# Kernel optimization log

Hardware: AMD Instinct MI355X
Metric: run time of the kernel (lower is better)

## Reference

```python
import jax, jax.numpy as jnp
import numpy as np

N_NODES = 15000
N_EDGES = 300000
N_RADIAL = 8
N_SPEC = 16
ZMAX = 64
CUTOFF = 5.0
LMAX = 2
NCHANNELS = 128


def bessel_basis(r, dim, rc):
    # b_n(r) = sqrt(2/rc) * sin(n*pi*r/rc) / r , n = 1..dim
    n = jnp.arange(1, dim + 1, dtype=r.dtype)
    return jnp.sqrt(2.0 / rc) * jnp.sin(n[None, :] * (jnp.pi / rc) * r[:, None]) / r[:, None]


def spherical_harmonics_l2(u):
    # Real solid harmonics of unit vectors up to l=2 (Racah/L2-style constants), 9 components
    x, y, z = u[:, 0], u[:, 1], u[:, 2]
    s3 = 3.0 ** 0.5
    s5 = 5.0 ** 0.5
    s15 = 15.0 ** 0.5
    one = jnp.ones_like(x)
    return jnp.stack([
        one,
        s3 * x, s3 * y, s3 * z,
        s15 * x * y, s15 * y * z,
        0.5 * s5 * (3.0 * z * z - 1.0),
        s15 * x * z, 0.5 * s15 * (x * x - y * y),
    ], axis=-1)  # [E, 9]


def setup_inputs() -> dict:
    key = jax.random.key(0)
    ks = jax.random.split(key, 8)
    vec = jax.random.normal(ks[0], (N_EDGES, 3), dtype=jnp.float32)
    distances = jnp.linalg.norm(vec, axis=-1) + 1e-3  # positive, consistent with vec
    switch = jax.random.uniform(ks[1], (N_EDGES,), dtype=jnp.float32)
    species_table = jax.random.normal(ks[2], (ZMAX, N_SPEC), dtype=jnp.float32)
    nbasis = N_RADIAL * N_SPEC
    W0 = jax.random.normal(ks[3], (nbasis, 2 * NCHANNELS), dtype=jnp.float32) / jnp.sqrt(nbasis)
    W1 = jax.random.normal(ks[4], (nbasis, 2 * NCHANNELS), dtype=jnp.float32) / jnp.sqrt(nbasis)
    W2 = jax.random.normal(ks[5], (nbasis, 2 * NCHANNELS), dtype=jnp.float32) / jnp.sqrt(nbasis)
    species = jax.random.randint(ks[6], (N_NODES,), 0, ZMAX)
    edge_src = jnp.sort(jax.random.randint(ks[7], (N_EDGES,), 0, N_NODES))
    edge_dst = jax.random.randint(jax.random.fold_in(key, 7), (N_EDGES,), 0, N_NODES)
    return {
        "distances": distances, "vec": vec, "switch": switch,
        "species_table": species_table, "W0": W0, "W1": W1, "W2": W2,
        "species": species, "edge_src": edge_src, "edge_dst": edge_dst,
    }


def reference(distances, vec, switch, species_table, W0, W1, W2, species, edge_src, edge_dst):
    n_nodes = species.shape[0]
    # radial basis * switch: [E, nr]
    rb = bessel_basis(distances, N_RADIAL, CUTOFF) * switch[:, None]
    senc = species_table[species]  # [N, ns]
    # edge-wise outer product radial x species -> [E, nr*ns]
    Dij = (rb[:, :, None] * senc[edge_dst, None, :]).reshape(rb.shape[0], -1)
    Y = spherical_harmonics_l2(vec / distances[:, None])  # [E, 9]
    # outer product with SH then scatter-sum to nodes: [N, 9, nbasis]
    rhoi = jax.ops.segment_sum(Dij[:, None, :] * Y[:, :, None], edge_src, num_segments=n_nodes)
    xis = [senc, rhoi[:, 0, :]]
    for l, W in enumerate((W0, W1, W2)):
        rhoil = rhoi[:, l * l:(l + 1) * (l + 1), :]  # [N, 2l+1, nbasis]
        xy = jnp.einsum('nmb,bc->nmc', rhoil, W)      # [N, 2l+1, 2*nchannels]
        xl, yl = jnp.split(xy, 2, axis=-1)
        xis.append((xl * yl).sum(axis=1) / (2 * l + 1) ** 0.5)
    return jnp.concatenate(xis, axis=-1)  # [N, ns + nbasis + 3*nchannels]
```

## Files before the change

kernel.cpp:

```cpp
#include <hip/hip_runtime.h>
#include <math.h>

#define N_NODES 15000
#define NPAD    15008
#define N_EDGES 300000
#define NCH     128
#define OUT_COLS 528
#define ES      300032
#define NCHUNK  (ES / 32)
#define CHROWS  72

typedef _Float16 half8   __attribute__((ext_vector_type(8)));
typedef short    short8  __attribute__((ext_vector_type(8)));
typedef float    floatx4 __attribute__((ext_vector_type(4)));

#define WF_BYTES    (3 * 256 * 128 * 2)
#define RP_OFF      WF_BYTES
#define RP_BYTES    61440
#define SPE_OFF     (RP_OFF + RP_BYTES)
#define SPE_BYTES   ((size_t)ES * 2)
#define AYT_OFF     (SPE_OFF + SPE_BYTES)
#define AYT_BYTES   ((size_t)NCHUNK * CHROWS * 32 * 2 + 4096)

#define PREP_EDGE_BLOCKS 1172
#define PREP_WF_BLOCKS   384
#define PREP_RP_BLOCKS   59
#define PREP_BLOCKS (PREP_EDGE_BLOCKS + PREP_WF_BLOCKS + PREP_RP_BLOCKS)

__device__ __forceinline__ size_t wf_pos(int l, int c, int k) {
    int h = c >> 7, cc = c & 127;
    int ct = cc >> 4, nI = cc & 15;
    int K = k >> 5, q = (k >> 3) & 3, j = k & 7;
    return ((size_t)((((l * 8 + ct) * 2 + h) * 4 + K) * 64 + q * 16 + nI)) * 8 + j;
}

__global__ __launch_bounds__(256) void prep_kernel(
    const float* __restrict__ dist, const float* __restrict__ vec,
    const float* __restrict__ sw,   const int* __restrict__ species,
    const int* __restrict__ edst,   const int* __restrict__ esrc,
    const float* __restrict__ W0, const float* __restrict__ W1,
    const float* __restrict__ W2,
    _Float16* __restrict__ AYt, short* __restrict__ spE,
    _Float16* __restrict__ WF,  int* __restrict__ row_ptr)
{
    const int b = blockIdx.x, tid = threadIdx.x;
    if (b < PREP_EDGE_BLOCKS) {
        int e = b * 256 + tid;
        if (e >= N_EDGES) return;

        const float bnorm = 0.6324555320336759f;
        const float s3  = 1.7320508075688772f;
        const float s5  = 2.2360679774997896f;
        const float s15 = 3.872983346207417f;
        const float cstep = 3.14159265358979323846f / 5.0f;

        float r    = dist[e];
        float invr = 1.0f / r;
        float g    = bnorm * invr * sw[e];
        float x = vec[3*e+0] * invr;
        float y = vec[3*e+1] * invr;
        float z = vec[3*e+2] * invr;

        spE[e] = (short)species[edst[e]];

        float f[8];
        #pragma unroll
        for (int n = 0; n < 8; ++n)
            f[n] = g * __sinf((float)(n + 1) * cstep * r);

        float Y[9];
        Y[0] = 1.0f;
        Y[1] = s3 * x;  Y[2] = s3 * y;  Y[3] = s3 * z;
        Y[4] = s15 * x * y;  Y[5] = s15 * y * z;
        Y[6] = 0.5f * s5 * (3.0f * z * z - 1.0f);
        Y[7] = s15 * x * z;  Y[8] = 0.5f * s15 * (x * x - y * y);

        _Float16* ab = AYt + (size_t)(e >> 5) * (CHROWS * 32) + (e & 31);
        #pragma unroll
        for (int m = 0; m < 9; ++m)
            #pragma unroll
            for (int n = 0; n < 8; ++n)
                ab[(m * 8 + n) * 32] = (_Float16)(Y[m] * f[n]);
    } else if (b < PREP_EDGE_BLOCKS + PREP_WF_BLOCKS) {
        int idx = (b - PREP_EDGE_BLOCKS) * 256 + tid;
        int l = idx >> 15;
        int c = (idx >> 7) & 255;
        int k = idx & 127;
        const float* W = (l == 0) ? W0 : ((l == 1) ? W1 : W2);
        WF[wf_pos(l, c, k)] = (_Float16)W[k * 256 + c];
    } else {
        int i = (b - PREP_EDGE_BLOCKS - PREP_WF_BLOCKS) * 256 + tid;
        if (i > NPAD) return;
        int lo = 0, hi = N_EDGES;
        while (lo < hi) { int mid = (lo + hi) >> 1; if (esrc[mid] < i) lo = mid + 1; else hi = mid; }
        row_ptr[i] = lo;
    }
}

__global__ __launch_bounds__(256) void main_kernel(
    const _Float16* __restrict__ AYt, const short* __restrict__ spE,
    const float* __restrict__ stab,  const int* __restrict__ row_ptr,
    const _Float16* __restrict__ WF, const int* __restrict__ species,
    float* __restrict__ out)
{
    __shared__ _Float16 stabL[64 * 16];
    __shared__ __align__(16) _Float16 srho[144 * 136];

    const int tid  = threadIdx.x;
    const int wave = tid >> 6;
    const int lane = tid & 63;
    const int q    = lane >> 4;
    const int nI   = lane & 15;
    const int node0 = blockIdx.x * 16;

    #pragma unroll
    for (int j = 0; j < 4; ++j) stabL[tid * 4 + j] = (_Float16)stab[tid * 4 + j];
    __syncthreads();

    for (int i = 0; i < 4; ++i) {
        const int n16 = 4 * wave + i;
        const int node = node0 + n16;
        const int lo = row_ptr[node], hi = row_ptr[node + 1];

        floatx4 acc[5];
        #pragma unroll
        for (int t = 0; t < 5; ++t) acc[t] = (floatx4){0.f, 0.f, 0.f, 0.f};

        for (int k0 = (lo & ~31); k0 < hi; k0 += 32) {
            short8 sp8 = *(const short8*)(spE + k0 + q * 8);
            half8 bfr;
            #pragma unroll
            for (int j = 0; j < 8; ++j) {
                int e = k0 + q * 8 + j;
                bool valid = (e >= lo) && (e < hi);
                int spv = valid ? (int)sp8[j] : 0;
                _Float16 v = stabL[spv * 16 + nI];
                bfr[j] = valid ? v : (_Float16)0;
            }
            const _Float16* cb = AYt + (size_t)(k0 >> 5) * (CHROWS * 32) + q * 8;
            #pragma unroll
            for (int t = 0; t < 5; ++t) {
                half8 a = *(const half8*)(cb + (t * 16 + nI) * 32);
                acc[t] = __builtin_amdgcn_mfma_f32_16x16x32_f16(a, bfr, acc[t], 0, 0, 0);
            }
        }

        #pragma unroll
        for (int t = 0; t < 5; ++t)
            #pragma unroll
            for (int r = 0; r < 4; ++r) {
                int row = t * 16 + q * 4 + r;
                if (row < 72) {
                    int m = row >> 3, nrad = row & 7;
                    int k = nrad * 16 + nI;
                    int K = k >> 5, qq = (k >> 3) & 3, j = k & 7;
                    srho[((m * 4 + K) * 4 + qq) * 136 + n16 * 8 + j] = (_Float16)acc[t][r];
                }
            }
    }
    __syncthreads();

    {
        int nn = tid >> 4, c = tid & 15;
        int node = node0 + nn;
        if (node < N_NODES) {
            float* o = out + (size_t)node * OUT_COLS;
            o[c] = stab[species[node] * 16 + c];
            int c0 = c * 8;
            int K = c0 >> 5, qq = (c0 >> 3) & 3;
            half8 h = *(const half8*)&srho[(K * 4 + qq) * 136 + nn * 8];
            #pragma unroll
            for (int j = 0; j < 8; ++j) o[16 + c0 + j] = (float)h[j];
        }
    }

    const int   mstart[3] = {0, 1, 4};
    const int   mcount[3] = {1, 3, 5};
    const float scl[3] = {1.0f, 0.5773502691896258f, 0.4472135954999579f};

    #pragma unroll
    for (int l = 0; l < 3; ++l) {
        half8 Bf[2][2][4];
        #pragma unroll
        for (int cp = 0; cp < 2; ++cp)
            #pragma unroll
            for (int h = 0; h < 2; ++h) {
                int ct = 2 * wave + cp;
                const _Float16* bp = WF +
                    ((size_t)((((l * 8 + ct) * 2 + h) * 4) * 64 + lane)) * 8;
                #pragma unroll
                for (int K = 0; K < 4; ++K)
                    Bf[cp][h][K] = *(const half8*)(bp + (size_t)K * 512);
            }

        floatx4 P0 = {0.f, 0.f, 0.f, 0.f};
        floatx4 P1 = {0.f, 0.f, 0.f, 0.f};

        #pragma unroll
        for (int mi = 0; mi < mcount[l]; ++mi) {
            int m = mstart[l] + mi;
            half8 Af[4];
            #pragma unroll
            for (int K = 0; K < 4; ++K)
                Af[K] = *(const half8*)&srho[((m * 4 + K) * 4 + q) * 136 + nI * 8];

            #pragma unroll
            for (int cp = 0; cp < 2; ++cp) {
                floatx4 Cx = {0.f, 0.f, 0.f, 0.f};
                floatx4 Cy = {0.f, 0.f, 0.f, 0.f};
                #pragma unroll
                for (int K = 0; K < 4; ++K) {
                    Cx = __builtin_amdgcn_mfma_f32_16x16x32_f16(Af[K], Bf[cp][0][K], Cx, 0, 0, 0);
                    Cy = __builtin_amdgcn_mfma_f32_16x16x32_f16(Af[K], Bf[cp][1][K], Cy, 0, 0, 0);
                }
                if (cp == 0) P0 += Cx * Cy; else P1 += Cx * Cy;
            }
        }

        #pragma unroll
        for (int cp = 0; cp < 2; ++cp) {
            floatx4 P = cp ? P1 : P0;
            int c = 144 + l * NCH + 16 * (2 * wave + cp) + nI;
            #pragma unroll
            for (int r = 0; r < 4; ++r) {
                int node = node0 + q * 4 + r;
                if (node < N_NODES)
                    out[(size_t)node * OUT_COLS + c] = P[r] * scl[l];
            }
        }
    }
}

extern "C" void kernel_launch(void* const* d_in, const int* in_sizes, int n_in,
                              void* d_out, int out_size, void* d_ws, size_t ws_size,
                              hipStream_t stream) {
    const float* distances = (const float*)d_in[0];
    const float* vec       = (const float*)d_in[1];
    const float* sw        = (const float*)d_in[2];
    const float* stab      = (const float*)d_in[3];
    const float* W0        = (const float*)d_in[4];
    const float* W1        = (const float*)d_in[5];
    const float* W2        = (const float*)d_in[6];
    const int*   species   = (const int*)d_in[7];
    const int*   esrc      = (const int*)d_in[8];
    const int*   edst      = (const int*)d_in[9];
    float* out = (float*)d_out;

    _Float16* WF     = (_Float16*)d_ws;
    int*      rowptr = (int*)((char*)d_ws + RP_OFF);
    short*    spE    = (short*)((char*)d_ws + SPE_OFF);
    _Float16* AYt    = (_Float16*)((char*)d_ws + AYT_OFF);

    prep_kernel<<<PREP_BLOCKS, 256, 0, stream>>>(
        distances, vec, sw, species, edst, esrc, W0, W1, W2,
        AYt, spE, WF, rowptr);
    main_kernel<<<NPAD / 16, 256, 0, stream>>>(
        AYt, spE, stab, rowptr, WF, species, out);
}
```

Before: 123.7 us.

## Store factored SH and radial values per edge; form products inside main kernel

```diff
diff --git a/kernel.cpp b/kernel.cpp
--- a/kernel.cpp
+++ b/kernel.cpp
@@ -8,7 +8,8 @@
 #define OUT_COLS 528
 #define ES      300032
 #define NCHUNK  (ES / 32)
-#define CHROWS  72
+#define YROWS   17
+#define CHB     (YROWS * 32)
 
 typedef _Float16 half8   __attribute__((ext_vector_type(8)));
 typedef short    short8  __attribute__((ext_vector_type(8)));
@@ -19,8 +20,8 @@
 #define RP_BYTES    61440
 #define SPE_OFF     (RP_OFF + RP_BYTES)
 #define SPE_BYTES   ((size_t)ES * 2)
-#define AYT_OFF     (SPE_OFF + SPE_BYTES)
-#define AYT_BYTES   ((size_t)NCHUNK * CHROWS * 32 * 2 + 4096)
+#define YF_OFF      (SPE_OFF + SPE_BYTES)
+#define YF_BYTES    ((size_t)NCHUNK * CHB * 2 + 256)
 
 #define PREP_EDGE_BLOCKS 1172
 #define PREP_WF_BLOCKS   384
@@ -40,7 +41,7 @@
     const int* __restrict__ edst,   const int* __restrict__ esrc,
     const float* __restrict__ W0, const float* __restrict__ W1,
     const float* __restrict__ W2,
-    _Float16* __restrict__ AYt, short* __restrict__ spE,
+    _Float16* __restrict__ Yf, short* __restrict__ spE,
     _Float16* __restrict__ WF,  int* __restrict__ row_ptr)
 {
     const int b = blockIdx.x, tid = threadIdx.x;
@@ -63,24 +64,19 @@
 
         spE[e] = (short)species[edst[e]];
 
-        float f[8];
+        _Float16* yb = Yf + (size_t)(e >> 5) * CHB + (e & 31);
+        yb[0 * 32] = (_Float16)1.0f;
+        yb[1 * 32] = (_Float16)(s3 * x);
+        yb[2 * 32] = (_Float16)(s3 * y);
+        yb[3 * 32] = (_Float16)(s3 * z);
+        yb[4 * 32] = (_Float16)(s15 * x * y);
+        yb[5 * 32] = (_Float16)(s15 * y * z);
+        yb[6 * 32] = (_Float16)(0.5f * s5 * (3.0f * z * z - 1.0f));
+        yb[7 * 32] = (_Float16)(s15 * x * z);
+        yb[8 * 32] = (_Float16)(0.5f * s15 * (x * x - y * y));
         #pragma unroll
         for (int n = 0; n < 8; ++n)
-            f[n] = g * __sinf((float)(n + 1) * cstep * r);
-
-        float Y[9];
-        Y[0] = 1.0f;
-        Y[1] = s3 * x;  Y[2] = s3 * y;  Y[3] = s3 * z;
-        Y[4] = s15 * x * y;  Y[5] = s15 * y * z;
-        Y[6] = 0.5f * s5 * (3.0f * z * z - 1.0f);
-        Y[7] = s15 * x * z;  Y[8] = 0.5f * s15 * (x * x - y * y);
-
-        _Float16* ab = AYt + (size_t)(e >> 5) * (CHROWS * 32) + (e & 31);
-        #pragma unroll
-        for (int m = 0; m < 9; ++m)
-            #pragma unroll
-            for (int n = 0; n < 8; ++n)
-                ab[(m * 8 + n) * 32] = (_Float16)(Y[m] * f[n]);
+            yb[(9 + n) * 32] = (_Float16)(g * __sinf((float)(n + 1) * cstep * r));
     } else if (b < PREP_EDGE_BLOCKS + PREP_WF_BLOCKS) {
         int idx = (b - PREP_EDGE_BLOCKS) * 256 + tid;
         int l = idx >> 15;
@@ -98,7 +94,7 @@
 }
 
 __global__ __launch_bounds__(256) void main_kernel(
-    const _Float16* __restrict__ AYt, const short* __restrict__ spE,
+    const _Float16* __restrict__ Yf, const short* __restrict__ spE,
     const float* __restrict__ stab,  const int* __restrict__ row_ptr,
     const _Float16* __restrict__ WF, const int* __restrict__ species,
     float* __restrict__ out)
@@ -137,10 +133,15 @@
                 _Float16 v = stabL[spv * 16 + nI];
                 bfr[j] = valid ? v : (_Float16)0;
             }
-            const _Float16* cb = AYt + (size_t)(k0 >> 5) * (CHROWS * 32) + q * 8;
+            const _Float16* yb = Yf + (size_t)(k0 >> 5) * CHB + q * 8;
             #pragma unroll
             for (int t = 0; t < 5; ++t) {
-                half8 a = *(const half8*)(cb + (t * 16 + nI) * 32);
+                int row = t * 16 + nI;
+                int m = row >> 3;
+                int n = row & 7;
+                half8 Y8 = *(const half8*)(yb + m * 32);
+                half8 F8 = *(const half8*)(yb + (9 + n) * 32);
+                half8 a = Y8 * F8;
                 acc[t] = __builtin_amdgcn_mfma_f32_16x16x32_f16(a, bfr, acc[t], 0, 0, 0);
             }
         }
@@ -249,11 +250,11 @@
     _Float16* WF     = (_Float16*)d_ws;
     int*      rowptr = (int*)((char*)d_ws + RP_OFF);
     short*    spE    = (short*)((char*)d_ws + SPE_OFF);
-    _Float16* AYt    = (_Float16*)((char*)d_ws + AYT_OFF);
+    _Float16* Yf     = (_Float16*)((char*)d_ws + YF_OFF);
 
     prep_kernel<<<PREP_BLOCKS, 256, 0, stream>>>(
         distances, vec, sw, species, edst, esrc, W0, W1, W2,
-        AYt, spE, WF, rowptr);
+        Yf, spE, WF, rowptr);
     main_kernel<<<NPAD / 16, 256, 0, stream>>>(
-        AYt, spE, stab, rowptr, WF, species, out);
-}
+        Yf, spE, stab, rowptr, WF, species, out);
+}
```

Measured after the change: 116.8 us. 1.06x faster.
